# Performance work log

Measured on AMD Instinct MI355X. Metric: run time of the kernel, lower is better.

Reference implementation:

```python
import jax, jax.numpy as jnp
import numpy as np

B, S, E, L, H, FF, CB = 16, 1000, 512, 4, 8, 2048, 4096
DH = E // H

def _ln(x, g, b):
    m = x.mean(-1, keepdims=True)
    v = ((x - m) ** 2).mean(-1, keepdims=True)
    return (x - m) / jnp.sqrt(v + 1e-5) * g + b

def setup_inputs() -> dict:
    key = jax.random.key(0)
    cnt = [0]
    def rn(shape, s=0.02):
        cnt[0] += 1
        return jax.random.normal(jax.random.fold_in(key, cnt[0]), shape, jnp.float32) * s
    inp = {}
    inp['noisy_tokens'] = jax.random.randint(jax.random.fold_in(key, 999), (B, S), 0, CB, dtype=jnp.int32)
    inp['codebook'] = rn((CB, E), 1.0)
    # sinusoidal positional encoding, as in _create_positional_encoding
    pe = np.zeros((S, E), np.float32)
    pos = np.arange(S, dtype=np.float32)[:, None]
    div = np.exp(np.arange(0, E, 2, dtype=np.float32) * (-np.log(10000.0) / E))
    pe[:, 0::2] = np.sin(pos * div)
    pe[:, 1::2] = np.cos(pos * div)
    inp['pos_enc'] = jnp.asarray(pe)[None]  # [1,S,E]
    # transformer encoder layers (stacked over L)
    inp['qkv_w'] = rn((L, 3 * E, E)); inp['qkv_b'] = jnp.zeros((L, 3 * E))
    inp['out_w'] = rn((L, E, E));     inp['out_b'] = jnp.zeros((L, E))
    inp['ln1_g'] = jnp.ones((L, E));  inp['ln1_b'] = jnp.zeros((L, E))
    inp['ln2_g'] = jnp.ones((L, E));  inp['ln2_b'] = jnp.zeros((L, E))
    inp['ff1_w'] = rn((L, FF, E));    inp['ff1_b'] = jnp.zeros((L, FF))
    inp['ff2_w'] = rn((L, E, FF));    inp['ff2_b'] = jnp.zeros((L, E))
    inp['fin_g'] = jnp.ones((E,));    inp['fin_b'] = jnp.zeros((E,))
    # post_process: Linear, LN, GELU, Linear
    inp['pp1_w'] = rn((E, E)); inp['pp1_b'] = jnp.zeros((E,))
    inp['pp_ln_g'] = jnp.ones((E,)); inp['pp_ln_b'] = jnp.zeros((E,))
    inp['pp2_w'] = rn((E, E)); inp['pp2_b'] = jnp.zeros((E,))
    inp['res_w'] = jnp.float32(0.1)
    # feature_to_codebook: Linear, LN, GELU, Linear (codebook_dim == E)
    inp['fc1_w'] = rn((E, E)); inp['fc1_b'] = jnp.zeros((E,))
    inp['fc_ln_g'] = jnp.ones((E,)); inp['fc_ln_b'] = jnp.zeros((E,))
    inp['fc2_w'] = rn((E, E)); inp['fc2_b'] = jnp.zeros((E,))
    return inp

def reference(noisy_tokens, codebook, pos_enc, qkv_w, qkv_b, out_w, out_b,
              ln1_g, ln1_b, ln2_g, ln2_b, ff1_w, ff1_b, ff2_w, ff2_b,
              fin_g, fin_b, pp1_w, pp1_b, pp_ln_g, pp_ln_b, pp2_w, pp2_b,
              res_w, fc1_w, fc1_b, fc_ln_g, fc_ln_b, fc2_w, fc2_b):
    gelu = lambda z: jax.nn.gelu(z, approximate=False)
    # token embedding (codebook_projection is Identity) + positional encoding
    x = codebook[noisy_tokens] + pos_enc            # [B,S,E]
    # pre-norm transformer encoder (dropout=0 / eval)
    y = x
    for l in range(L):
        h = _ln(y, ln1_g[l], ln1_b[l])
        qkv = h @ qkv_w[l].T + qkv_b[l]             # [B,S,3E]
        q, k, v = jnp.split(qkv, 3, axis=-1)
        q = q.reshape(B, S, H, DH); k = k.reshape(B, S, H, DH); v = v.reshape(B, S, H, DH)
        scores = jnp.einsum('bqhd,bkhd->bhqk', q, k) / jnp.sqrt(jnp.float32(DH))
        attn = jax.nn.softmax(scores, axis=-1)
        ctx = jnp.einsum('bhqk,bkhd->bqhd', attn, v).reshape(B, S, E)
        y = y + (ctx @ out_w[l].T + out_b[l])
        h2 = _ln(y, ln2_g[l], ln2_b[l])
        y = y + (gelu(h2 @ ff1_w[l].T + ff1_b[l]) @ ff2_w[l].T + ff2_b[l])
    y = _ln(y, fin_g, fin_b)
    # post_process + residual
    pp = gelu(_ln(y @ pp1_w.T + pp1_b, pp_ln_g, pp_ln_b)) @ pp2_w.T + pp2_b
    enhanced = x + res_w * pp
    # feature_to_codebook
    fc = gelu(_ln(enhanced @ fc1_w.T + fc1_b, fc_ln_g, fc_ln_b)) @ fc2_w.T + fc2_b  # [B,S,E]
    # quantize: nearest neighbour in codebook (cdist + argmin)
    flat = fc.reshape(-1, E)
    d2 = (jnp.sum(flat ** 2, -1, keepdims=True)
          - 2.0 * flat @ codebook.T
          + jnp.sum(codebook ** 2, -1))            # [B*S, CB]
    tokens = jnp.argmin(d2, axis=-1).reshape(B, S)
    return fc, tokens
```

## Files before the change

kernel.cpp:

```cpp
#include <hip/hip_runtime.h>
#include <hip/hip_bf16.h>
#include <math.h>

#define NTOK 16000
#define E    512
#define FFD  2048
#define CBN  4096
#define SEQ  1000
#define NH   8
#define VLD  1008

typedef __hip_bfloat16 bf16;
typedef __attribute__((ext_vector_type(8))) short short8;
typedef __attribute__((ext_vector_type(4))) float f32x4;

__device__ __forceinline__ float gelu_f(float v) {
    return 0.5f * v * (1.0f + erff(v * 0.70710678118654752f));
}

__device__ __forceinline__ void split_store(float v, bf16* hi, bf16* lo, size_t idx) {
    bf16 h = __float2bfloat16(v);
    hi[idx] = h;
    lo[idx] = __float2bfloat16(v - __bfloat162float(h));
}

__device__ __forceinline__ void gll16(const bf16* g, short* l) {
    __builtin_amdgcn_global_load_lds((const __attribute__((address_space(1))) void*)g,
                                     (__attribute__((address_space(3))) void*)l, 16, 0, 0);
}

__device__ __forceinline__ void t2_ins(float v, int c, float& v1, int& c1, float& v2, int& c2) {
    const bool b1 = (v < v1) || (v == v1 && c < c1);
    const bool b2 = (v < v2) || (v == v2 && c < c2);
    if (b1) { v2 = v1; c2 = c1; v1 = v; c1 = c; }
    else if (b2) { v2 = v; c2 = c; }
}

__global__ __launch_bounds__(128) void embed_kernel(const int* __restrict__ tok,
                                                    const float* __restrict__ cb,
                                                    const float* __restrict__ pe,
                                                    float* __restrict__ y) {
    const int row = blockIdx.x;
    const int s = row % SEQ;
    const int t = tok[row];
    const int c = threadIdx.x * 4;
    const float4 cv = *(const float4*)(cb + (size_t)t * E + c);
    const float4 pv = *(const float4*)(pe + (size_t)s * E + c);
    *(float4*)(y + (size_t)row * E + c) =
        make_float4(cv.x + pv.x, cv.y + pv.y, cv.z + pv.z, cv.w + pv.w);
}

__global__ __launch_bounds__(256) void split_w(const float* __restrict__ src, int ld,
                                               int cols_log2, int n,
                                               bf16* __restrict__ hi, bf16* __restrict__ lo) {
    const int i = blockIdx.x * 256 + threadIdx.x;
    if (i >= n) return;
    const int r = i >> cols_log2;
    const int c = i & ((1 << cols_log2) - 1);
    const float v = src[(size_t)r * ld + c];
    split_store(v, hi, lo, i);
}

template<int GELU>
__global__ __launch_bounds__(256) void ln_planes(const float* __restrict__ in,
                                                 bf16* __restrict__ hi, bf16* __restrict__ lo,
                                                 const float* __restrict__ g,
                                                 const float* __restrict__ b) {
    const int lane = threadIdx.x & 63;
    const int row = blockIdx.x * 4 + (threadIdx.x >> 6);
    const float* p = in + (size_t)row * E;
    const float4 v0 = *(const float4*)(p + lane * 4);
    const float4 v1 = *(const float4*)(p + 256 + lane * 4);
    float sum = v0.x + v0.y + v0.z + v0.w + v1.x + v1.y + v1.z + v1.w;
    float sq = v0.x * v0.x + v0.y * v0.y + v0.z * v0.z + v0.w * v0.w
             + v1.x * v1.x + v1.y * v1.y + v1.z * v1.z + v1.w * v1.w;
#pragma unroll
    for (int m = 1; m < 64; m <<= 1) {
        sum += __shfl_xor(sum, m);
        sq += __shfl_xor(sq, m);
    }
    const float mean = sum * (1.0f / 512.0f);
    const float var = sq * (1.0f / 512.0f) - mean * mean;
    const float rstd = rsqrtf(var + 1e-5f);
    const float4 g0 = *(const float4*)(g + lane * 4);
    const float4 g1 = *(const float4*)(g + 256 + lane * 4);
    const float4 b0 = *(const float4*)(b + lane * 4);
    const float4 b1 = *(const float4*)(b + 256 + lane * 4);
    const size_t base = (size_t)row * E;
    float o;
    const float vv0[4] = {v0.x, v0.y, v0.z, v0.w};
    const float gg0[4] = {g0.x, g0.y, g0.z, g0.w};
    const float bb0[4] = {b0.x, b0.y, b0.z, b0.w};
    const float vv1[4] = {v1.x, v1.y, v1.z, v1.w};
    const float gg1[4] = {g1.x, g1.y, g1.z, g1.w};
    const float bb1[4] = {b1.x, b1.y, b1.z, b1.w};
#pragma unroll
    for (int t = 0; t < 4; ++t) {
        o = (vv0[t] - mean) * rstd * gg0[t] + bb0[t];
        if (GELU) o = gelu_f(o);
        split_store(o, hi, lo, base + lane * 4 + t);
        o = (vv1[t] - mean) * rstd * gg1[t] + bb1[t];
        if (GELU) o = gelu_f(o);
        split_store(o, hi, lo, base + 256 + lane * 4 + t);
    }
}

template<int OUT>
__global__ __launch_bounds__(256) void gemm_split(
    const bf16* __restrict__ Ah, const bf16* __restrict__ Al, int lda,
    const bf16* __restrict__ Wh, const bf16* __restrict__ Wl, int ldw,
    const float* __restrict__ bias,
    float* __restrict__ C, int ldc,
    bf16* __restrict__ Ohi, bf16* __restrict__ Olo, int ldp,
    const int* __restrict__ noisy, const float* __restrict__ cb,
    const float* __restrict__ pe, const float* __restrict__ resw,
    int K) {
    __shared__ __align__(16) short planes[4][128][32];
    const int tid = threadIdx.x;
    const int rowBase = blockIdx.y * 128;
    const int colBase = blockIdx.x * 128;
    const int wave = tid >> 6, lane = tid & 63;
    const int wm = (wave & 1) * 64, wn = (wave >> 1) * 64;
    const int lm = lane & 15;
    const int psl8 = ((lane >> 4) ^ ((lm >> 1) & 3)) * 8;

    const bf16* src = (wave == 0) ? Ah : (wave == 1) ? Al : (wave == 2) ? Wh : Wl;
    const int sld = (wave < 2) ? lda : ldw;
    const int srb = (wave < 2) ? rowBase : colBase;
    const int sslot = (lane & 3) ^ ((lane >> 3) & 3);
    const bf16* sp = src + (size_t)(srb + (lane >> 2)) * sld + sslot * 8;
    short* lb = &planes[wave][0][0];

    f32x4 acc[4][4];
#pragma unroll
    for (int i = 0; i < 4; ++i)
#pragma unroll
        for (int j = 0; j < 4; ++j)
            acc[i][j] = (f32x4){0.f, 0.f, 0.f, 0.f};

    for (int k0 = 0; k0 < K; k0 += 32) {
        __syncthreads();
        {
            const bf16* p = sp + k0;
#pragma unroll
            for (int j = 0; j < 8; ++j)
                gll16(p + (size_t)j * 16 * sld, lb + j * 512);
        }
        __syncthreads();
        short8 ah[4], al[4], wh[4], wl[4];
#pragma unroll
        for (int i = 0; i < 4; ++i) {
            ah[i] = *(const short8*)&planes[0][wm + i * 16 + lm][psl8];
            al[i] = *(const short8*)&planes[1][wm + i * 16 + lm][psl8];
            wh[i] = *(const short8*)&planes[2][wn + i * 16 + lm][psl8];
            wl[i] = *(const short8*)&planes[3][wn + i * 16 + lm][psl8];
        }
#pragma unroll
        for (int i = 0; i < 4; ++i)
#pragma unroll
            for (int j = 0; j < 4; ++j)
                acc[i][j] = __builtin_amdgcn_mfma_f32_16x16x32_bf16(ah[i], wh[j], acc[i][j], 0, 0, 0);
#pragma unroll
        for (int i = 0; i < 4; ++i)
#pragma unroll
            for (int j = 0; j < 4; ++j)
                acc[i][j] = __builtin_amdgcn_mfma_f32_16x16x32_bf16(ah[i], wl[j], acc[i][j], 0, 0, 0);
#pragma unroll
        for (int i = 0; i < 4; ++i)
#pragma unroll
            for (int j = 0; j < 4; ++j)
                acc[i][j] = __builtin_amdgcn_mfma_f32_16x16x32_bf16(al[i], wh[j], acc[i][j], 0, 0, 0);
    }

    float bv[4];
#pragma unroll
    for (int j = 0; j < 4; ++j)
        bv[j] = bias ? bias[colBase + wn + j * 16 + lm] : 0.f;
    float scv = 0.f;
    if (OUT == 3) scv = resw[0];
#pragma unroll
    for (int i = 0; i < 4; ++i) {
#pragma unroll
        for (int reg = 0; reg < 4; ++reg) {
            const int r = rowBase + wm + i * 16 + (lane >> 4) * 4 + reg;
            int tok = 0, srow = 0;
            if (OUT == 3) { tok = noisy[r]; srow = r % SEQ; }
#pragma unroll
            for (int j = 0; j < 4; ++j) {
                const int col = colBase + wn + j * 16 + lm;
                float v = acc[i][j][reg] + bv[j];
                if (OUT == 0) {
                    C[(size_t)r * ldc + col] = v;
                } else if (OUT == 1) {
                    float* cp = C + (size_t)r * ldc + col;
                    *cp = *cp + v;
                } else if (OUT == 2) {
                    v = gelu_f(v);
                    split_store(v, Ohi, Olo, (size_t)r * ldp + col);
                } else if (OUT == 3) {
                    const float xv = cb[(size_t)tok * E + col] + pe[(size_t)srow * E + col];
                    v = xv + scv * v;
                    split_store(v, Ohi, Olo, (size_t)r * ldp + col);
                } else if (OUT == 4) {
                    split_store(v, Ohi, Olo, (size_t)r * ldp + col);
                } else {
                    C[(size_t)r * ldc + col] = v;
                    split_store(v, Ohi, Olo, (size_t)r * ldp + col);
                }
            }
        }
    }
}

__global__ __launch_bounds__(256) void vtrans(const bf16* __restrict__ vh_src,
                                              const bf16* __restrict__ vl_src,
                                              bf16* __restrict__ vth,
                                              bf16* __restrict__ vtl) {
    __shared__ short T[64][72];
    const int tid = threadIdx.x;
    const int st = blockIdx.x;
    const int bh = blockIdx.y;
    const int b = bh >> 3, h = bh & 7;
    const int sr = tid >> 2, dq = (tid & 3) * 16;
    const int s_g = st * 64 + sr;
    const int od = tid >> 3;
    const int osq = (tid & 7) * 8;
#pragma unroll
    for (int p = 0; p < 2; ++p) {
        const short* src = (const short*)(p ? vl_src : vh_src);
        short* dst = (short*)(p ? vtl : vth);
        short8 a0 = {0, 0, 0, 0, 0, 0, 0, 0};
        short8 a1 = {0, 0, 0, 0, 0, 0, 0, 0};
        if (s_g < SEQ) {
            const short* sp = src + (size_t)(b * SEQ + s_g) * 1536 + 1024 + h * 64 + dq;
            a0 = *(const short8*)sp;
            a1 = *(const short8*)(sp + 8);
        }
        __syncthreads();
#pragma unroll
        for (int j = 0; j < 8; ++j) T[dq + j][sr] = a0[j];
#pragma unroll
        for (int j = 0; j < 8; ++j) T[dq + 8 + j][sr] = a1[j];
        __syncthreads();
        const int scol = st * 64 + osq;
        if (scol + 8 <= VLD) {
            const short8 o0 = *(const short8*)&T[od][osq];
            const short8 o1 = *(const short8*)&T[od + 32][osq];
            *(short8*)(dst + (size_t)(bh * 64 + od) * VLD + scol) = o0;
            *(short8*)(dst + (size_t)(bh * 64 + od + 32) * VLD + scol) = o1;
        }
    }
}

__global__ __launch_bounds__(256) void attn_mfma(const bf16* __restrict__ qkh,
                                                 const bf16* __restrict__ qkl,
                                                 const bf16* __restrict__ vth,
                                                 const bf16* __restrict__ vtl,
                                                 bf16* __restrict__ chi,
                                                 bf16* __restrict__ clo) {
    __shared__ short QPs[2][64][72];
    __shared__ short Ks[2][64][72];
    __shared__ short Vs[2][64][72];
    const int tid = threadIdx.x;
    const int qt = blockIdx.x, bh = blockIdx.y;
    const int b = bh >> 3, h = bh & 7;
    const int wave = tid >> 6, lane = tid & 63;
    const int lm = lane & 15, g = lane >> 4, q8 = g * 8;
    const int wq = wave * 16;
    const int r0 = tid >> 2, kq = (tid & 3) * 16;

    {
        const int q = qt * 64 + r0;
        short8 z = {0, 0, 0, 0, 0, 0, 0, 0};
        short8 a0 = z, a1 = z, b0 = z, b1 = z;
        if (q < SEQ) {
            const size_t base = (size_t)(b * SEQ + q) * 1536 + h * 64 + kq;
            a0 = *(const short8*)((const short*)qkh + base);
            a1 = *(const short8*)((const short*)qkh + base + 8);
            b0 = *(const short8*)((const short*)qkl + base);
            b1 = *(const short8*)((const short*)qkl + base + 8);
        }
        *(short8*)&QPs[0][r0][kq] = a0; *(short8*)&QPs[0][r0][kq + 8] = a1;
        *(short8*)&QPs[1][r0][kq] = b0; *(short8*)&QPs[1][r0][kq + 8] = b1;
    }
    __syncthreads();
    short8 qfh[2], qfl[2];
#pragma unroll
    for (int t = 0; t < 2; ++t) {
        qfh[t] = *(const short8*)&QPs[0][wq + lm][t * 32 + q8];
        qfl[t] = *(const short8*)&QPs[1][wq + lm][t * 32 + q8];
    }

    float m_i[4] = {-3e38f, -3e38f, -3e38f, -3e38f};
    float l_i[4] = {0.f, 0.f, 0.f, 0.f};
    f32x4 o[4];
#pragma unroll
    for (int dt = 0; dt < 4; ++dt) o[dt] = (f32x4){0.f, 0.f, 0.f, 0.f};

    for (int kb = 0; kb < SEQ; kb += 64) {
        __syncthreads();
        {
            const int kr = kb + r0;
            short8 z = {0, 0, 0, 0, 0, 0, 0, 0};
            short8 a0 = z, a1 = z, b0 = z, b1 = z;
            if (kr < SEQ) {
                const size_t base = (size_t)(b * SEQ + kr) * 1536 + 512 + h * 64 + kq;
                a0 = *(const short8*)((const short*)qkh + base);
                a1 = *(const short8*)((const short*)qkh + base + 8);
                b0 = *(const short8*)((const short*)qkl + base);
                b1 = *(const short8*)((const short*)qkl + base + 8);
            }
            *(short8*)&Ks[0][r0][kq] = a0; *(short8*)&Ks[0][r0][kq + 8] = a1;
            *(short8*)&Ks[1][r0][kq] = b0; *(short8*)&Ks[1][r0][kq + 8] = b1;
            const size_t vbase = (size_t)(bh * 64 + r0) * VLD + kb + kq;
            short8 v0 = z, v1 = z, w0 = z, w1 = z;
            if (kb + kq + 8 <= VLD) {
                v0 = *(const short8*)((const short*)vth + vbase);
                w0 = *(const short8*)((const short*)vtl + vbase);
            }
            if (kb + kq + 16 <= VLD) {
                v1 = *(const short8*)((const short*)vth + vbase + 8);
                w1 = *(const short8*)((const short*)vtl + vbase + 8);
            }
            *(short8*)&Vs[0][r0][kq] = v0; *(short8*)&Vs[0][r0][kq + 8] = v1;
            *(short8*)&Vs[1][r0][kq] = w0; *(short8*)&Vs[1][r0][kq + 8] = w1;
        }
        __syncthreads();
        f32x4 sac[4];
#pragma unroll
        for (int j = 0; j < 4; ++j) sac[j] = (f32x4){0.f, 0.f, 0.f, 0.f};
#pragma unroll
        for (int t = 0; t < 2; ++t) {
#pragma unroll
            for (int j = 0; j < 4; ++j) {
                const short8 kh = *(const short8*)&Ks[0][j * 16 + lm][t * 32 + q8];
                const short8 kl = *(const short8*)&Ks[1][j * 16 + lm][t * 32 + q8];
                sac[j] = __builtin_amdgcn_mfma_f32_16x16x32_bf16(qfh[t], kh, sac[j], 0, 0, 0);
                sac[j] = __builtin_amdgcn_mfma_f32_16x16x32_bf16(qfh[t], kl, sac[j], 0, 0, 0);
                sac[j] = __builtin_amdgcn_mfma_f32_16x16x32_bf16(qfl[t], kh, sac[j], 0, 0, 0);
            }
        }
        float alpha_v[4];
#pragma unroll
        for (int reg = 0; reg < 4; ++reg) {
            float sv[4];
            float rm = -3e38f;
#pragma unroll
            for (int j = 0; j < 4; ++j) {
                const int kc = kb + j * 16 + lm;
                float s = sac[j][reg] * 0.125f;
                s = (kc < SEQ) ? s : -3e38f;
                sv[j] = s;
                rm = fmaxf(rm, s);
            }
#pragma unroll
            for (int m = 1; m < 16; m <<= 1) rm = fmaxf(rm, __shfl_xor(rm, m));
            const float mn = fmaxf(m_i[reg], rm);
            const float al = expf(m_i[reg] - mn);
            float rs = 0.f;
            const int prow = wq + g * 4 + reg;
#pragma unroll
            for (int j = 0; j < 4; ++j) {
                const float pv = expf(sv[j] - mn);
                rs += pv;
                bf16 phb = __float2bfloat16(pv);
                bf16 plb = __float2bfloat16(pv - __bfloat162float(phb));
                QPs[0][prow][j * 16 + lm] = *reinterpret_cast<short*>(&phb);
                QPs[1][prow][j * 16 + lm] = *reinterpret_cast<short*>(&plb);
            }
#pragma unroll
            for (int m = 1; m < 16; m <<= 1) rs += __shfl_xor(rs, m);
            l_i[reg] = l_i[reg] * al + rs;
            m_i[reg] = mn;
            alpha_v[reg] = al;
        }
        const f32x4 av = {alpha_v[0], alpha_v[1], alpha_v[2], alpha_v[3]};
#pragma unroll
        for (int dt = 0; dt < 4; ++dt) o[dt] *= av;
        __syncthreads();
#pragma unroll
        for (int t = 0; t < 2; ++t) {
            const short8 ph = *(const short8*)&QPs[0][wq + lm][t * 32 + q8];
            const short8 pl = *(const short8*)&QPs[1][wq + lm][t * 32 + q8];
#pragma unroll
            for (int dt = 0; dt < 4; ++dt) {
                const short8 vh = *(const short8*)&Vs[0][dt * 16 + lm][t * 32 + q8];
                const short8 vl = *(const short8*)&Vs[1][dt * 16 + lm][t * 32 + q8];
                o[dt] = __builtin_amdgcn_mfma_f32_16x16x32_bf16(ph, vh, o[dt], 0, 0, 0);
                o[dt] = __builtin_amdgcn_mfma_f32_16x16x32_bf16(ph, vl, o[dt], 0, 0, 0);
                o[dt] = __builtin_amdgcn_mfma_f32_16x16x32_bf16(pl, vh, o[dt], 0, 0, 0);
            }
        }
    }
#pragma unroll
    for (int reg = 0; reg < 4; ++reg) {
        const int q = qt * 64 + wq + g * 4 + reg;
        if (q < SEQ) {
            const float inv = 1.0f / l_i[reg];
#pragma unroll
            for (int dt = 0; dt < 4; ++dt) {
                const size_t idx = (size_t)(b * SEQ + q) * E + h * 64 + dt * 16 + lm;
                split_store(o[dt][reg] * inv, chi, clo, idx);
            }
        }
    }
}

__global__ __launch_bounds__(256) void cbnorm_kernel(const float* __restrict__ cb,
                                                     float* __restrict__ out) {
    const int lane = threadIdx.x & 63;
    const int row = blockIdx.x * 4 + (threadIdx.x >> 6);
    const float* p = cb + (size_t)row * E;
    const float4 v0 = *(const float4*)(p + lane * 4);
    const float4 v1 = *(const float4*)(p + 256 + lane * 4);
    float sq = v0.x * v0.x + v0.y * v0.y + v0.z * v0.z + v0.w * v0.w
             + v1.x * v1.x + v1.y * v1.y + v1.z * v1.z + v1.w * v1.w;
#pragma unroll
    for (int m = 1; m < 64; m <<= 1) sq += __shfl_xor(sq, m);
    if (lane == 0) out[row] = sq;
}

__global__ __launch_bounds__(256) void argmin_mfma(
    const bf16* __restrict__ Ah, const bf16* __restrict__ Al,
    const bf16* __restrict__ Wh, const bf16* __restrict__ Wl,
    const float* __restrict__ cbn, float4* __restrict__ part) {
    __shared__ __align__(16) short smem[17408];
    float4* mrg = reinterpret_cast<float4*>(smem);
    const int tid = threadIdx.x;
    const int rowBase = blockIdx.y * 128;
    const int wave = tid >> 6, lane = tid & 63;
    const int wm = wave * 32;
    const int lm = lane & 15;
    const int g = lane >> 4;
    const int psl8 = (g ^ ((lm >> 1) & 3)) * 8;
    const int own_row = tid >> 1;
    const int own_half = tid & 1;

    const bf16* ssrc = (wave == 0) ? Ah : (wave == 1) ? Al : (wave == 2) ? Wh : Wl;
    const int sslot = (lane & 3) ^ ((lane >> 3) & 3);
    short* lb = smem + wave * 4096;

    float rv1 = 3e38f, rv2 = 3e38f;
    int rc1 = 0x7fffffff, rc2 = 0x7fffffff;

    for (int ct = 0; ct < 4; ++ct) {
        const int colBase = blockIdx.x * 512 + ct * 128;
        const int rb = (wave < 2) ? rowBase : colBase;
        const bf16* sp = ssrc + (size_t)(rb + (lane >> 2)) * E + sslot * 8;
        f32x4 acc[2][8];
#pragma unroll
        for (int i = 0; i < 2; ++i)
#pragma unroll
            for (int j = 0; j < 8; ++j)
                acc[i][j] = (f32x4){0.f, 0.f, 0.f, 0.f};

        for (int k0 = 0; k0 < E; k0 += 32) {
            __syncthreads();
            {
                const bf16* p = sp + k0;
#pragma unroll
                for (int j = 0; j < 8; ++j)
                    gll16(p + (size_t)j * 16 * E, lb + j * 512);
            }
            __syncthreads();
            short8 ah[2], al2[2], wh[8], wl[8];
#pragma unroll
            for (int i = 0; i < 2; ++i) {
                ah[i]  = *(const short8*)(smem + 0 * 4096 + (wm + i * 16 + lm) * 32 + psl8);
                al2[i] = *(const short8*)(smem + 1 * 4096 + (wm + i * 16 + lm) * 32 + psl8);
            }
#pragma unroll
            for (int j = 0; j < 8; ++j) {
                wh[j] = *(const short8*)(smem + 2 * 4096 + (j * 16 + lm) * 32 + psl8);
                wl[j] = *(const short8*)(smem + 3 * 4096 + (j * 16 + lm) * 32 + psl8);
            }
#pragma unroll
            for (int i = 0; i < 2; ++i)
#pragma unroll
                for (int j = 0; j < 8; ++j)
                    acc[i][j] = __builtin_amdgcn_mfma_f32_16x16x32_bf16(ah[i], wh[j], acc[i][j], 0, 0, 0);
#pragma unroll
            for (int i = 0; i < 2; ++i)
#pragma unroll
                for (int j = 0; j < 8; ++j)
                    acc[i][j] = __builtin_amdgcn_mfma_f32_16x16x32_bf16(ah[i], wl[j], acc[i][j], 0, 0, 0);
#pragma unroll
            for (int i = 0; i < 2; ++i)
#pragma unroll
                for (int j = 0; j < 8; ++j)
                    acc[i][j] = __builtin_amdgcn_mfma_f32_16x16x32_bf16(al2[i], wh[j], acc[i][j], 0, 0, 0);
        }

        float nv[8];
#pragma unroll
        for (int j = 0; j < 8; ++j) nv[j] = cbn[colBase + j * 16 + lm];
        __syncthreads();
#pragma unroll
        for (int i = 0; i < 2; ++i) {
#pragma unroll
            for (int reg = 0; reg < 4; ++reg) {
                const int row_local = wm + i * 16 + g * 4 + reg;
                float v1 = 3e38f, v2 = 3e38f;
                int c1 = 0x7fffffff, c2 = 0x7fffffff;
#pragma unroll
                for (int j = 0; j < 8; ++j) {
                    const float d = nv[j] - 2.0f * acc[i][j][reg];
                    t2_ins(d, colBase + j * 16 + lm, v1, c1, v2, c2);
                }
                mrg[row_local * 17 + lm] = make_float4(v1, (float)c1, v2, (float)c2);
            }
        }
        __syncthreads();
        {
            float mv1 = 3e38f, mv2 = 3e38f;
            int mc1 = 0x7fffffff, mc2 = 0x7fffffff;
#pragma unroll
            for (int e = 0; e < 8; ++e) {
                const float4 p = mrg[own_row * 17 + own_half * 8 + e];
                t2_ins(p.x, (int)p.y, mv1, mc1, mv2, mc2);
                t2_ins(p.z, (int)p.w, mv1, mc1, mv2, mc2);
            }
            const float pv1 = __shfl_xor(mv1, 1); const int pc1 = __shfl_xor(mc1, 1);
            const float pv2 = __shfl_xor(mv2, 1); const int pc2 = __shfl_xor(mc2, 1);
            t2_ins(pv1, pc1, mv1, mc1, mv2, mc2);
            t2_ins(pv2, pc2, mv1, mc1, mv2, mc2);
            t2_ins(mv1, mc1, rv1, rc1, rv2, rc2);
            t2_ins(mv2, mc2, rv1, rc1, rv2, rc2);
        }
    }
    if (own_half == 0)
        part[(size_t)(rowBase + own_row) * 8 + blockIdx.x] =
            make_float4(rv1, (float)rc1, rv2, (float)rc2);
}

__global__ __launch_bounds__(256) void argmin_exact(const float4* __restrict__ part,
                                                    const float* __restrict__ fc,
                                                    const float* __restrict__ cb,
                                                    const float* __restrict__ cbn,
                                                    float* __restrict__ tokf) {
    const int wave = threadIdx.x >> 6, lane = threadIdx.x & 63;
    const int r = blockIdx.x * 4 + wave;
    float v1 = 3e38f, v2 = 3e38f;
    int c1 = 0x7fffffff, c2 = 0x7fffffff;
    if (lane < 8) {
        const float4 p = part[(size_t)r * 8 + lane];
        v1 = p.x; c1 = (int)p.y; v2 = p.z; c2 = (int)p.w;
    }
#pragma unroll
    for (int m = 1; m < 8; m <<= 1) {
        const float w1 = __shfl_xor(v1, m); const int d1i = __shfl_xor(c1, m);
        const float w2 = __shfl_xor(v2, m); const int d2i = __shfl_xor(c2, m);
        t2_ins(w1, d1i, v1, c1, v2, c2);
        t2_ins(w2, d2i, v1, c1, v2, c2);
    }
    c1 = __shfl(c1, 0);
    c2 = __shfl(c2, 0);
    const float* fr = fc + (size_t)r * E + lane * 8;
    const float* p1 = cb + (size_t)c1 * E + lane * 8;
    const float* p2 = cb + (size_t)c2 * E + lane * 8;
    float d1 = 0.f, d2 = 0.f;
#pragma unroll
    for (int j = 0; j < 8; ++j) {
        const float f = fr[j];
        d1 += f * p1[j];
        d2 += f * p2[j];
    }
#pragma unroll
    for (int m = 1; m < 64; m <<= 1) {
        d1 += __shfl_xor(d1, m);
        d2 += __shfl_xor(d2, m);
    }
    d1 = cbn[c1] - 2.0f * d1;
    d2 = cbn[c2] - 2.0f * d2;
    const int win = ((d1 < d2) || (d1 == d2 && c1 < c2)) ? c1 : c2;
    if (lane == 0) tokf[r] = (float)win;
}

extern "C" void kernel_launch(void* const* d_in, const int* in_sizes, int n_in,
                              void* d_out, int out_size, void* d_ws, size_t ws_size,
                              hipStream_t stream) {
    const int* noisy = (const int*)d_in[0];
    const float* codebook = (const float*)d_in[1];
    const float* pos_enc = (const float*)d_in[2];
    const float* qkv_w = (const float*)d_in[3];
    const float* qkv_b = (const float*)d_in[4];
    const float* out_w = (const float*)d_in[5];
    const float* out_b = (const float*)d_in[6];
    const float* ln1_g = (const float*)d_in[7];
    const float* ln1_b = (const float*)d_in[8];
    const float* ln2_g = (const float*)d_in[9];
    const float* ln2_b = (const float*)d_in[10];
    const float* ff1_w = (const float*)d_in[11];
    const float* ff1_b = (const float*)d_in[12];
    const float* ff2_w = (const float*)d_in[13];
    const float* ff2_b = (const float*)d_in[14];
    const float* fin_g = (const float*)d_in[15];
    const float* fin_b = (const float*)d_in[16];
    const float* pp1_w = (const float*)d_in[17];
    const float* pp1_b = (const float*)d_in[18];
    const float* pp_ln_g = (const float*)d_in[19];
    const float* pp_ln_b = (const float*)d_in[20];
    const float* pp2_w = (const float*)d_in[21];
    const float* pp2_b = (const float*)d_in[22];
    const float* res_w = (const float*)d_in[23];
    const float* fc1_w = (const float*)d_in[24];
    const float* fc1_b = (const float*)d_in[25];
    const float* fc_ln_g = (const float*)d_in[26];
    const float* fc_ln_b = (const float*)d_in[27];
    const float* fc2_w = (const float*)d_in[28];
    const float* fc2_b = (const float*)d_in[29];

    float* ws = (float*)d_ws;
    float* y = ws;
    float* REG = ws + 8192000;
    bf16* qkvh = (bf16*)REG;
    bf16* qkvl = qkvh + 24576000;
    bf16* mid_hi = (bf16*)REG;
    bf16* mid_lo = mid_hi + 16384000;
    float* slotA = REG;
    float* slotB = REG + 8192000;
    bf16* e_hi = (bf16*)slotA;
    bf16* e_lo = e_hi + 8192000;
    bf16* fcp2_hi = (bf16*)(REG + 16384000);
    bf16* fcp2_lo = fcp2_hi + 8192000;
    float* WV = ws + 32768000;
    bf16* vth = (bf16*)WV;
    bf16* vtl = vth + 8192 * VLD;
    bf16* wA_hi = (bf16*)WV;
    bf16* wA_lo = wA_hi + 1048576;
    bf16* wB_hi = wA_lo + 1048576;
    bf16* wB_lo = wB_hi + 1048576;
    bf16* cbh = wB_lo + 1048576;
    bf16* cbl = cbh + 2097152;
    float* cbn = slotB;
    float4* part = (float4*)(slotB + 4096);
    bf16* h_hi = (bf16*)d_out;
    bf16* h_lo = h_hi + 8192000;
    float* tokf = (float*)d_out + 8192000;

    const dim3 blk(256);
    const dim3 g512(4, 125), g1024(8, 125), g1536(12, 125);

    embed_kernel<<<dim3(NTOK), dim3(128), 0, stream>>>(noisy, codebook, pos_enc, y);

    for (int l = 0; l < 4; ++l) {
        ln_planes<0><<<dim3(4000), blk, 0, stream>>>(y, h_hi, h_lo, ln1_g + l * E, ln1_b + l * E);
        split_w<<<dim3(3072), blk, 0, stream>>>(qkv_w + (size_t)l * 1536 * E, E, 9, 1536 * E, wA_hi, wA_lo);
        gemm_split<4><<<g1536, blk, 0, stream>>>(
            h_hi, h_lo, E, wA_hi, wA_lo, E, qkv_b + (size_t)l * 1536,
            nullptr, 0, qkvh, qkvl, 1536, nullptr, nullptr, nullptr, nullptr, E);
        vtrans<<<dim3(16, 128), blk, 0, stream>>>(qkvh, qkvl, vth, vtl);
        attn_mfma<<<dim3(16, 128), blk, 0, stream>>>(qkvh, qkvl, vth, vtl, h_hi, h_lo);
        split_w<<<dim3(1024), blk, 0, stream>>>(out_w + (size_t)l * E * E, E, 9, E * E, wB_hi, wB_lo);
        gemm_split<1><<<g512, blk, 0, stream>>>(
            h_hi, h_lo, E, wB_hi, wB_lo, E, out_b + (size_t)l * E,
            y, E, nullptr, nullptr, 0, nullptr, nullptr, nullptr, nullptr, E);
        ln_planes<0><<<dim3(4000), blk, 0, stream>>>(y, h_hi, h_lo, ln2_g + l * E, ln2_b + l * E);
        split_w<<<dim3(4096), blk, 0, stream>>>(ff1_w + (size_t)l * FFD * E, E, 9, FFD * E, wA_hi, wA_lo);
        split_w<<<dim3(4096), blk, 0, stream>>>(ff2_w + (size_t)l * E * FFD, FFD, 11, E * FFD, wB_hi, wB_lo);
        for (int c = 0; c < 2; ++c) {
            gemm_split<2><<<g1024, blk, 0, stream>>>(
                h_hi, h_lo, E, wA_hi + (size_t)c * 1024 * E, wA_lo + (size_t)c * 1024 * E, E,
                ff1_b + (size_t)l * FFD + c * 1024,
                nullptr, 0, mid_hi, mid_lo, 1024, nullptr, nullptr, nullptr, nullptr, E);
            gemm_split<1><<<g512, blk, 0, stream>>>(
                mid_hi, mid_lo, 1024, wB_hi + c * 1024, wB_lo + c * 1024, FFD,
                (c == 0) ? (ff2_b + (size_t)l * E) : nullptr,
                y, E, nullptr, nullptr, 0, nullptr, nullptr, nullptr, nullptr, 1024);
        }
    }

    ln_planes<0><<<dim3(4000), blk, 0, stream>>>(y, h_hi, h_lo, fin_g, fin_b);
    split_w<<<dim3(1024), blk, 0, stream>>>(pp1_w, E, 9, E * E, wA_hi, wA_lo);
    gemm_split<0><<<g512, blk, 0, stream>>>(
        h_hi, h_lo, E, wA_hi, wA_lo, E, pp1_b,
        slotB, E, nullptr, nullptr, 0, nullptr, nullptr, nullptr, nullptr, E);
    ln_planes<1><<<dim3(4000), blk, 0, stream>>>(slotB, h_hi, h_lo, pp_ln_g, pp_ln_b);
    split_w<<<dim3(1024), blk, 0, stream>>>(pp2_w, E, 9, E * E, wB_hi, wB_lo);
    gemm_split<3><<<g512, blk, 0, stream>>>(
        h_hi, h_lo, E, wB_hi, wB_lo, E, pp2_b,
        nullptr, 0, e_hi, e_lo, E, noisy, codebook, pos_enc, res_w, E);
    split_w<<<dim3(1024), blk, 0, stream>>>(fc1_w, E, 9, E * E, wA_hi, wA_lo);
    gemm_split<0><<<g512, blk, 0, stream>>>(
        e_hi, e_lo, E, wA_hi, wA_lo, E, fc1_b,
        slotB, E, nullptr, nullptr, 0, nullptr, nullptr, nullptr, nullptr, E);
    ln_planes<1><<<dim3(4000), blk, 0, stream>>>(slotB, h_hi, h_lo, fc_ln_g, fc_ln_b);
    split_w<<<dim3(1024), blk, 0, stream>>>(fc2_w, E, 9, E * E, wB_hi, wB_lo);
    gemm_split<5><<<g512, blk, 0, stream>>>(
        h_hi, h_lo, E, wB_hi, wB_lo, E, fc2_b,
        slotA, E, fcp2_hi, fcp2_lo, E, nullptr, nullptr, nullptr, nullptr, E);

    split_w<<<dim3(8192), blk, 0, stream>>>(codebook, E, 9, CBN * E, cbh, cbl);
    cbnorm_kernel<<<dim3(1024), blk, 0, stream>>>(codebook, cbn);
    argmin_mfma<<<dim3(8, 125), blk, 0, stream>>>(fcp2_hi, fcp2_lo, cbh, cbl, cbn, part);
    argmin_exact<<<dim3(4000), blk, 0, stream>>>(part, slotA, codebook, cbn, tokf);
    hipMemcpyAsync(d_out, slotA, (size_t)8192000 * 4, hipMemcpyDeviceToDevice, stream);
}
```

Baseline: 3.785 ms.

## Double-buffer LDS tiles in split GEMMs and prefetch K/V in attention

Converts the split-bf16 GEMM and the fused codebook-distance GEMM main loops to double-buffered LDS. The next K-slice is issued with direct global-to-LDS loads while MFMAs run on the current buffer, leaving one barrier per iteration instead of two. The attention kernel now loads the next K/V tile into registers right after the LDS store barrier, so global latency overlaps with compute. The argmin merge buffer switches from padded stride 17 to an XOR-swizzled stride 16 so it fits the doubled LDS footprint, at the cost of twice the GEMM LDS usage and possibly lower occupancy.

```diff
diff --git a/kernel.cpp b/kernel.cpp
--- a/kernel.cpp
+++ b/kernel.cpp
@@ -115,7 +115,7 @@
     const int* __restrict__ noisy, const float* __restrict__ cb,
     const float* __restrict__ pe, const float* __restrict__ resw,
     int K) {
-    __shared__ __align__(16) short planes[4][128][32];
+    __shared__ __align__(16) short SB[2][4][128][32];
     const int tid = threadIdx.x;
     const int rowBase = blockIdx.y * 128;
     const int colBase = blockIdx.x * 128;
@@ -129,7 +129,8 @@
     const int srb = (wave < 2) ? rowBase : colBase;
     const int sslot = (lane & 3) ^ ((lane >> 3) & 3);
     const bf16* sp = src + (size_t)(srb + (lane >> 2)) * sld + sslot * 8;
-    short* lb = &planes[wave][0][0];
+    short* lb0 = &SB[0][wave][0][0];
+    short* lb1 = &SB[1][wave][0][0];
 
     f32x4 acc[4][4];
 #pragma unroll
@@ -138,22 +139,30 @@
         for (int j = 0; j < 4; ++j)
             acc[i][j] = (f32x4){0.f, 0.f, 0.f, 0.f};
 
-    for (int k0 = 0; k0 < K; k0 += 32) {
-        __syncthreads();
-        {
-            const bf16* p = sp + k0;
+    const int nt = K >> 5;
+    {
+#pragma unroll
+        for (int j = 0; j < 8; ++j)
+            gll16(sp + (size_t)j * 16 * sld, lb0 + j * 512);
+    }
+    __syncthreads();
+    int cur = 0;
+    for (int t = 0; t < nt; ++t) {
+        if (t + 1 < nt) {
+            short* lb = cur ? lb0 : lb1;
+            const bf16* p = sp + (t + 1) * 32;
 #pragma unroll
             for (int j = 0; j < 8; ++j)
                 gll16(p + (size_t)j * 16 * sld, lb + j * 512);
         }
-        __syncthreads();
+        const short (*P)[128][32] = SB[cur];
         short8 ah[4], al[4], wh[4], wl[4];
 #pragma unroll
         for (int i = 0; i < 4; ++i) {
-            ah[i] = *(const short8*)&planes[0][wm + i * 16 + lm][psl8];
-            al[i] = *(const short8*)&planes[1][wm + i * 16 + lm][psl8];
-            wh[i] = *(const short8*)&planes[2][wn + i * 16 + lm][psl8];
-            wl[i] = *(const short8*)&planes[3][wn + i * 16 + lm][psl8];
+            ah[i] = *(const short8*)&P[0][wm + i * 16 + lm][psl8];
+            al[i] = *(const short8*)&P[1][wm + i * 16 + lm][psl8];
+            wh[i] = *(const short8*)&P[2][wn + i * 16 + lm][psl8];
+            wl[i] = *(const short8*)&P[3][wn + i * 16 + lm][psl8];
         }
 #pragma unroll
         for (int i = 0; i < 4; ++i)
@@ -170,6 +179,8 @@
 #pragma unroll
             for (int j = 0; j < 4; ++j)
                 acc[i][j] = __builtin_amdgcn_mfma_f32_16x16x32_bf16(al[i], wh[j], acc[i][j], 0, 0, 0);
+        __syncthreads();
+        cur ^= 1;
     }
 
     float bv[4];
@@ -268,10 +279,10 @@
     const int lm = lane & 15, g = lane >> 4, q8 = g * 8;
     const int wq = wave * 16;
     const int r0 = tid >> 2, kq = (tid & 3) * 16;
+    const short8 z = {0, 0, 0, 0, 0, 0, 0, 0};
 
     {
         const int q = qt * 64 + r0;
-        short8 z = {0, 0, 0, 0, 0, 0, 0, 0};
         short8 a0 = z, a1 = z, b0 = z, b1 = z;
         if (q < SEQ) {
             const size_t base = (size_t)(b * SEQ + q) * 1536 + h * 64 + kq;
@@ -297,35 +308,41 @@
 #pragma unroll
     for (int dt = 0; dt < 4; ++dt) o[dt] = (f32x4){0.f, 0.f, 0.f, 0.f};
 
+    short8 ka0 = z, ka1 = z, kl0 = z, kl1 = z;
+    short8 va0 = z, va1 = z, vl0 = z, vl1 = z;
+    auto loadKV = [&](int kb2) {
+        const int kr = kb2 + r0;
+        ka0 = z; ka1 = z; kl0 = z; kl1 = z;
+        if (kr < SEQ) {
+            const size_t base = (size_t)(b * SEQ + kr) * 1536 + 512 + h * 64 + kq;
+            ka0 = *(const short8*)((const short*)qkh + base);
+            ka1 = *(const short8*)((const short*)qkh + base + 8);
+            kl0 = *(const short8*)((const short*)qkl + base);
+            kl1 = *(const short8*)((const short*)qkl + base + 8);
+        }
+        const size_t vbase = (size_t)(bh * 64 + r0) * VLD + kb2 + kq;
+        va0 = z; va1 = z; vl0 = z; vl1 = z;
+        if (kb2 + kq + 8 <= VLD) {
+            va0 = *(const short8*)((const short*)vth + vbase);
+            vl0 = *(const short8*)((const short*)vtl + vbase);
+        }
+        if (kb2 + kq + 16 <= VLD) {
+            va1 = *(const short8*)((const short*)vth + vbase + 8);
+            vl1 = *(const short8*)((const short*)vtl + vbase + 8);
+        }
+    };
+    loadKV(0);
+
     for (int kb = 0; kb < SEQ; kb += 64) {
         __syncthreads();
         {
-            const int kr = kb + r0;
-            short8 z = {0, 0, 0, 0, 0, 0, 0, 0};
-            short8 a0 = z, a1 = z, b0 = z, b1 = z;
-            if (kr < SEQ) {
-                const size_t base = (size_t)(b * SEQ + kr) * 1536 + 512 + h * 64 + kq;
-                a0 = *(const short8*)((const short*)qkh + base);
-                a1 = *(const short8*)((const short*)qkh + base + 8);
-                b0 = *(const short8*)((const short*)qkl + base);
-                b1 = *(const short8*)((const short*)qkl + base + 8);
-            }
-            *(short8*)&Ks[0][r0][kq] = a0; *(short8*)&Ks[0][r0][kq + 8] = a1;
-            *(short8*)&Ks[1][r0][kq] = b0; *(short8*)&Ks[1][r0][kq + 8] = b1;
-            const size_t vbase = (size_t)(bh * 64 + r0) * VLD + kb + kq;
-            short8 v0 = z, v1 = z, w0 = z, w1 = z;
-            if (kb + kq + 8 <= VLD) {
-                v0 = *(const short8*)((const short*)vth + vbase);
-                w0 = *(const short8*)((const short*)vtl + vbase);
-            }
-            if (kb + kq + 16 <= VLD) {
-                v1 = *(const short8*)((const short*)vth + vbase + 8);
-                w1 = *(const short8*)((const short*)vtl + vbase + 8);
-            }
-            *(short8*)&Vs[0][r0][kq] = v0; *(short8*)&Vs[0][r0][kq + 8] = v1;
-            *(short8*)&Vs[1][r0][kq] = w0; *(short8*)&Vs[1][r0][kq + 8] = w1;
-        }
-        __syncthreads();
+            *(short8*)&Ks[0][r0][kq] = ka0; *(short8*)&Ks[0][r0][kq + 8] = ka1;
+            *(short8*)&Ks[1][r0][kq] = kl0; *(short8*)&Ks[1][r0][kq + 8] = kl1;
+            *(short8*)&Vs[0][r0][kq] = va0; *(short8*)&Vs[0][r0][kq + 8] = va1;
+            *(short8*)&Vs[1][r0][kq] = vl0; *(short8*)&Vs[1][r0][kq + 8] = vl1;
+        }
+        __syncthreads();
+        if (kb + 64 < SEQ) loadKV(kb + 64);
         f32x4 sac[4];
 #pragma unroll
         for (int j = 0; j < 4; ++j) sac[j] = (f32x4){0.f, 0.f, 0.f, 0.f};
@@ -424,8 +441,8 @@
     const bf16* __restrict__ Ah, const bf16* __restrict__ Al,
     const bf16* __restrict__ Wh, const bf16* __restrict__ Wl,
     const float* __restrict__ cbn, float4* __restrict__ part) {
-    __shared__ __align__(16) short smem[17408];
-    float4* mrg = reinterpret_cast<float4*>(smem);
+    __shared__ __align__(16) short SB[2][4][128][32];
+    float4* mrg = reinterpret_cast<float4*>(&SB[0][0][0][0]);
     const int tid = threadIdx.x;
     const int rowBase = blockIdx.y * 128;
     const int wave = tid >> 6, lane = tid & 63;
@@ -438,7 +455,8 @@
 
     const bf16* ssrc = (wave == 0) ? Ah : (wave == 1) ? Al : (wave == 2) ? Wh : Wl;
     const int sslot = (lane & 3) ^ ((lane >> 3) & 3);
-    short* lb = smem + wave * 4096;
+    short* lb0 = &SB[0][wave][0][0];
+    short* lb1 = &SB[1][wave][0][0];
 
     float rv1 = 3e38f, rv2 = 3e38f;
     int rc1 = 0x7fffffff, rc2 = 0x7fffffff;
@@ -454,25 +472,33 @@
             for (int j = 0; j < 8; ++j)
                 acc[i][j] = (f32x4){0.f, 0.f, 0.f, 0.f};
 
-        for (int k0 = 0; k0 < E; k0 += 32) {
-            __syncthreads();
-            {
-                const bf16* p = sp + k0;
+        __syncthreads();
+        {
+#pragma unroll
+            for (int j = 0; j < 8; ++j)
+                gll16(sp + (size_t)j * 16 * E, lb0 + j * 512);
+        }
+        __syncthreads();
+        int cur = 0;
+        for (int t = 0; t < 16; ++t) {
+            if (t < 15) {
+                short* lb = cur ? lb0 : lb1;
+                const bf16* p = sp + (t + 1) * 32;
 #pragma unroll
                 for (int j = 0; j < 8; ++j)
                     gll16(p + (size_t)j * 16 * E, lb + j * 512);
             }
-            __syncthreads();
+            const short (*P)[128][32] = SB[cur];
             short8 ah[2], al2[2], wh[8], wl[8];
 #pragma unroll
             for (int i = 0; i < 2; ++i) {
-                ah[i]  = *(const short8*)(smem + 0 * 4096 + (wm + i * 16 + lm) * 32 + psl8);
-                al2[i] = *(const short8*)(smem + 1 * 4096 + (wm + i * 16 + lm) * 32 + psl8);
+                ah[i]  = *(const short8*)&P[0][wm + i * 16 + lm][psl8];
+                al2[i] = *(const short8*)&P[1][wm + i * 16 + lm][psl8];
             }
 #pragma unroll
             for (int j = 0; j < 8; ++j) {
-                wh[j] = *(const short8*)(smem + 2 * 4096 + (j * 16 + lm) * 32 + psl8);
-                wl[j] = *(const short8*)(smem + 3 * 4096 + (j * 16 + lm) * 32 + psl8);
+                wh[j] = *(const short8*)&P[2][j * 16 + lm][psl8];
+                wl[j] = *(const short8*)&P[3][j * 16 + lm][psl8];
             }
 #pragma unroll
             for (int i = 0; i < 2; ++i)
@@ -489,12 +515,13 @@
 #pragma unroll
                 for (int j = 0; j < 8; ++j)
                     acc[i][j] = __builtin_amdgcn_mfma_f32_16x16x32_bf16(al2[i], wh[j], acc[i][j], 0, 0, 0);
+            __syncthreads();
+            cur ^= 1;
         }
 
         float nv[8];
 #pragma unroll
         for (int j = 0; j < 8; ++j) nv[j] = cbn[colBase + j * 16 + lm];
-        __syncthreads();
 #pragma unroll
         for (int i = 0; i < 2; ++i) {
 #pragma unroll
@@ -507,7 +534,7 @@
                     const float d = nv[j] - 2.0f * acc[i][j][reg];
                     t2_ins(d, colBase + j * 16 + lm, v1, c1, v2, c2);
                 }
-                mrg[row_local * 17 + lm] = make_float4(v1, (float)c1, v2, (float)c2);
+                mrg[row_local * 16 + (lm ^ (row_local & 15))] = make_float4(v1, (float)c1, v2, (float)c2);
             }
         }
         __syncthreads();
@@ -516,7 +543,8 @@
             int mc1 = 0x7fffffff, mc2 = 0x7fffffff;
 #pragma unroll
             for (int e = 0; e < 8; ++e) {
-                const float4 p = mrg[own_row * 17 + own_half * 8 + e];
+                const int cc = own_half * 8 + e;
+                const float4 p = mrg[own_row * 16 + (cc ^ (own_row & 15))];
                 t2_ins(p.x, (int)p.y, mv1, mc1, mv2, mc2);
                 t2_ins(p.z, (int)p.w, mv1, mc1, mv2, mc2);
             }
```

Measured after the change: 3.587 ms. 5.2% less time.
